# Kernel tuning notes

Measured on AMD Instinct MI355X. Metric: run time of the kernel, lower is better.

## Reference

```python
import jax, jax.numpy as jnp
import numpy as np

N_NODES = 100000
N_EDGES = 640000
D_IN = 128
D_OUT = 128
D_HID = 128  # assumed MLP hidden width (repo MLP not shown; standard 2-layer GIN MLP)


def setup_inputs() -> dict:
    key = jax.random.key(0)
    k = jax.random.split(key, 8)
    x = jax.random.normal(k[0], (N_NODES, D_IN), dtype=jnp.float32)
    edge_index = jax.random.randint(k[1], (2, N_EDGES), 0, N_NODES, dtype=jnp.int64)
    edge_attr = jax.random.normal(k[2], (N_EDGES, D_IN), dtype=jnp.float32)
    # learned params
    eps = jnp.zeros((), dtype=jnp.float32)  # train_eps=True, init 0
    s1 = 1.0 / np.sqrt(D_IN)
    s2 = 1.0 / np.sqrt(D_HID)
    W1 = jax.random.uniform(k[3], (D_IN, D_HID), jnp.float32, -s1, s1)
    b1 = jax.random.uniform(k[4], (D_HID,), jnp.float32, -s1, s1)
    W2 = jax.random.uniform(k[5], (D_HID, D_OUT), jnp.float32, -s2, s2)
    b2 = jax.random.uniform(k[6], (D_OUT,), jnp.float32, -s2, s2)
    return {"x": x, "edge_index": edge_index, "edge_attr": edge_attr,
            "eps": eps, "W1": W1, "b1": b1, "W2": W2, "b2": b2}


def reference(x, edge_index, edge_attr, eps, W1, b1, W2, b2):
    src = edge_index[0]  # source nodes j
    dst = edge_index[1]  # target nodes i
    # message: ReLU(x_j + edge_attr)  -- [E, D_IN]
    msg = jax.nn.relu(x[src] + edge_attr)
    # scatter-sum aggregation to target nodes -- [N, D_IN]
    aggr = jax.ops.segment_sum(msg, dst, num_segments=N_NODES)
    # GINE update: (1 + eps) * x_i + aggr, then MLP (dropout=0.0 -> identity)
    h = (1.0 + eps) * x + aggr
    h = jax.nn.relu(h @ W1 + b1)
    out = h @ W2 + b2
    return out
```

## Files before the change

kernel.cpp:

```cpp
#include <hip/hip_runtime.h>

constexpr int NN = 100000;
constexpr int NE = 640000;
constexpr int D  = 128;
constexpr int NB = (NN + 255) / 256;

typedef __attribute__((ext_vector_type(8))) short bf16x8;
typedef __attribute__((ext_vector_type(4))) float f32x4;

__device__ __forceinline__ short f2bf(float f) {
    union { float f; unsigned u; } v; v.f = f;
    unsigned r = v.u + 0x7FFF + ((v.u >> 16) & 1);
    return (short)(r >> 16);
}
__device__ __forceinline__ float bf2f(short h) {
    union { unsigned u; float f; } v;
    v.u = ((unsigned)(unsigned short)h) << 16;
    return v.f;
}

__global__ __launch_bounds__(256) void k_zero(int* __restrict__ cnt) {
    int i = blockIdx.x * 256 + threadIdx.x;
    if (i < NN) cnt[i] = 0;
}

__global__ __launch_bounds__(256) void k_hist(const int* __restrict__ dst,
                                              int* __restrict__ cnt) {
    int e = blockIdx.x * 256 + threadIdx.x;
    if (e < NE) atomicAdd(&cnt[dst[e]], 1);
}

__global__ __launch_bounds__(256) void k_bsum(const int* __restrict__ cnt,
                                              int* __restrict__ bsum) {
    int i = blockIdx.x * 256 + threadIdx.x;
    int v = (i < NN) ? cnt[i] : 0;
#pragma unroll
    for (int s = 32; s; s >>= 1) v += __shfl_down(v, s, 64);
    __shared__ int w[4];
    if ((threadIdx.x & 63) == 0) w[threadIdx.x >> 6] = v;
    __syncthreads();
    if (threadIdx.x == 0) bsum[blockIdx.x] = w[0] + w[1] + w[2] + w[3];
}

__global__ __launch_bounds__(512) void k_scan_bsum(const int* __restrict__ bsum,
                                                   int* __restrict__ bboff) {
    int t = threadIdx.x, lane = t & 63;
    int v = (t < NB) ? bsum[t] : 0;
    int incl = v;
#pragma unroll
    for (int s = 1; s < 64; s <<= 1) {
        int u = __shfl_up(incl, s, 64);
        if (lane >= s) incl += u;
    }
    __shared__ int wt[8], wp[8];
    if (lane == 63) wt[t >> 6] = incl;
    __syncthreads();
    if (t == 0) { int run = 0; for (int i = 0; i < 8; ++i) { wp[i] = run; run += wt[i]; } }
    __syncthreads();
    if (t < NB) bboff[t] = incl - v + wp[t >> 6];
}

__global__ __launch_bounds__(256) void k_scan_final(const int* __restrict__ cnt,
                                                    const int* __restrict__ bboff,
                                                    int* __restrict__ off,
                                                    int* __restrict__ cur) {
    int b = blockIdx.x, t = threadIdx.x, lane = t & 63;
    int i = b * 256 + t;
    int v = (i < NN) ? cnt[i] : 0;
    int incl = v;
#pragma unroll
    for (int s = 1; s < 64; s <<= 1) {
        int u = __shfl_up(incl, s, 64);
        if (lane >= s) incl += u;
    }
    __shared__ int wt[4], wp[4];
    if (lane == 63) wt[t >> 6] = incl;
    __syncthreads();
    if (t == 0) { int run = 0; for (int q = 0; q < 4; ++q) { wp[q] = run; run += wt[q]; } }
    __syncthreads();
    int excl = incl - v + wp[t >> 6] + bboff[b];
    if (i < NN) { off[i] = excl; cur[i] = excl; }
    if (i == 0) off[NN] = NE;
}

__global__ __launch_bounds__(256) void k_perm(const int* __restrict__ dst,
                                              const int* __restrict__ src,
                                              int* __restrict__ cur,
                                              int2* __restrict__ ps) {
    int e = blockIdx.x * 256 + threadIdx.x;
    if (e < NE) {
        int p = atomicAdd(&cur[dst[e]], 1);
        int2 v; v.x = e; v.y = src[e];
        ps[p] = v;
    }
}

__global__ __launch_bounds__(256) void k_agg(const float* __restrict__ x,
                                             const float* __restrict__ ea,
                                             const int* __restrict__ off,
                                             const int2* __restrict__ ps,
                                             const float* __restrict__ eps,
                                             float* __restrict__ h) {
    int wave = threadIdx.x >> 6;
    int lane = threadIdx.x & 63;
    int n = blockIdx.x * 4 + wave;
    if (n >= NN) return;
    int j0 = off[n], j1 = off[n + 1];
    const int lo2 = lane * 2;
    float2 acc; acc.x = 0.0f; acc.y = 0.0f;

    for (int j = j0; j < j1; j += 8) {
        int ee[8], ss[8];
#pragma unroll
        for (int q = 0; q < 8; ++q) {
            int jj = j + q; jj = (jj < j1) ? jj : (j1 - 1);
            int2 p = ps[jj];
            ee[q] = p.x; ss[q] = p.y;
        }
        float2 xa[8], eb[8];
#pragma unroll
        for (int q = 0; q < 8; ++q) {
            xa[q] = *reinterpret_cast<const float2*>(x  + (size_t)ss[q] * D + lo2);
            eb[q] = *reinterpret_cast<const float2*>(ea + (size_t)ee[q] * D + lo2);
        }
#pragma unroll
        for (int q = 0; q < 8; ++q) {
            float mx = fmaxf(xa[q].x + eb[q].x, 0.0f);
            float my = fmaxf(xa[q].y + eb[q].y, 0.0f);
            bool ok = (j + q) < j1;
            acc.x += ok ? mx : 0.0f;
            acc.y += ok ? my : 0.0f;
        }
    }
    float sc = 1.0f + eps[0];
    float2 xx = *reinterpret_cast<const float2*>(x + (size_t)n * D + lo2);
    float2 o;
    o.x = fmaf(sc, xx.x, acc.x);
    o.y = fmaf(sc, xx.y, acc.y);
    *reinterpret_cast<float2*>(h + (size_t)n * D + lo2) = o;
}

template<bool RELU>
__global__ __launch_bounds__(256) void k_gemm(const float* __restrict__ A,
                                              const float* __restrict__ W,
                                              const float* __restrict__ bias,
                                              float* __restrict__ out) {
    constexpr int LDW = 136;
    __shared__ short Whi[128 * LDW];
    __shared__ short Wlo[128 * LDW];

    for (int idx = threadIdx.x; idx < 128 * 128; idx += 256) {
        int k = idx >> 7, n = idx & 127;
        float w = W[idx];
        short hi = f2bf(w);
        short lo = f2bf(w - bf2f(hi));
        Whi[n * LDW + k] = hi;
        Wlo[n * LDW + k] = lo;
    }
    __syncthreads();

    const int wave = threadIdx.x >> 6;
    const int lane = threadIdx.x & 63;
    const int r = lane & 15;
    const int g = lane >> 4;

    const long mb = (long)blockIdx.x * 128 + wave * 16;

    f32x4 acc[2][8];
#pragma unroll
    for (int mt = 0; mt < 2; ++mt)
#pragma unroll
        for (int nt = 0; nt < 8; ++nt) {
            acc[mt][nt].x = 0.f; acc[mt][nt].y = 0.f;
            acc[mt][nt].z = 0.f; acc[mt][nt].w = 0.f;
        }

#pragma unroll
    for (int kc = 0; kc < 4; ++kc) {
        const int k0 = kc * 32;
        bf16x8 ahi[2], alo[2];
#pragma unroll
        for (int mt = 0; mt < 2; ++mt) {
            long row = mb + mt * 64 + r;
            row = (row < NN) ? row : (NN - 1);
            const float* ap = A + row * D + k0 + g * 8;
            float4 v0 = reinterpret_cast<const float4*>(ap)[0];
            float4 v1 = reinterpret_cast<const float4*>(ap)[1];
            float vals[8] = {v0.x, v0.y, v0.z, v0.w, v1.x, v1.y, v1.z, v1.w};
#pragma unroll
            for (int i = 0; i < 8; ++i) {
                short hb = f2bf(vals[i]);
                ahi[mt][i] = hb;
                alo[mt][i] = f2bf(vals[i] - bf2f(hb));
            }
        }
#pragma unroll
        for (int nt = 0; nt < 8; ++nt) {
            const int wb = (nt * 16 + r) * LDW + k0 + g * 8;
            bf16x8 whi = *reinterpret_cast<const bf16x8*>(&Whi[wb]);
            bf16x8 wlo = *reinterpret_cast<const bf16x8*>(&Wlo[wb]);
#pragma unroll
            for (int mt = 0; mt < 2; ++mt) {
                acc[mt][nt] = __builtin_amdgcn_mfma_f32_16x16x32_bf16(ahi[mt], whi, acc[mt][nt], 0, 0, 0);
                acc[mt][nt] = __builtin_amdgcn_mfma_f32_16x16x32_bf16(ahi[mt], wlo, acc[mt][nt], 0, 0, 0);
                acc[mt][nt] = __builtin_amdgcn_mfma_f32_16x16x32_bf16(alo[mt], whi, acc[mt][nt], 0, 0, 0);
            }
        }
    }

#pragma unroll
    for (int nt = 0; nt < 8; ++nt) {
        const int col = nt * 16 + r;
        const float bb = bias[col];
#pragma unroll
        for (int mt = 0; mt < 2; ++mt) {
#pragma unroll
            for (int q = 0; q < 4; ++q) {
                long row = mb + mt * 64 + g * 4 + q;
                if (row < NN) {
                    float v = acc[mt][nt][q] + bb;
                    if (RELU) v = fmaxf(v, 0.0f);
                    out[row * D + col] = v;
                }
            }
        }
    }
}

extern "C" void kernel_launch(void* const* d_in, const int* in_sizes, int n_in,
                              void* d_out, int out_size, void* d_ws, size_t ws_size,
                              hipStream_t stream) {
    const float* x   = (const float*)d_in[0];
    const int*   ei  = (const int*)d_in[1];
    const float* ea  = (const float*)d_in[2];
    const float* eps = (const float*)d_in[3];
    const float* W1  = (const float*)d_in[4];
    const float* b1  = (const float*)d_in[5];
    const float* W2  = (const float*)d_in[6];
    const float* b2  = (const float*)d_in[7];
    float* out = (float*)d_out;

    const int* src = ei;
    const int* dst = ei + NE;

    int* base  = (int*)d_ws;
    int* cnt   = base;
    int* off   = cnt + NN;
    int* cur   = off + NN + 1;
    int* bsum  = cur + NN;
    int* bboff = bsum + NB;
    size_t ps_off = ((size_t)(3 * NN + 1 + 2 * NB) + 1) & ~(size_t)1;
    int2* ps   = (int2*)(base + ps_off);
    float* g   = (float*)d_ws;

    k_zero      <<<NB,               256, 0, stream>>>(cnt);
    k_hist      <<<(NE + 255) / 256, 256, 0, stream>>>(dst, cnt);
    k_bsum      <<<NB,               256, 0, stream>>>(cnt, bsum);
    k_scan_bsum <<<1,                512, 0, stream>>>(bsum, bboff);
    k_scan_final<<<NB,               256, 0, stream>>>(cnt, bboff, off, cur);
    k_perm      <<<(NE + 255) / 256, 256, 0, stream>>>(dst, src, cur, ps);

    k_agg<<<(NN + 3) / 4, 256, 0, stream>>>(x, ea, off, ps, eps, out);
    k_gemm<true> <<<(NN + 127) / 128, 256, 0, stream>>>(out, W1, b1, g);
    k_gemm<false><<<(NN + 127) / 128, 256, 0, stream>>>(g, W2, b2, out);
}
```

Baseline: 305.9 us.

## Fuse two MLP GEMMs into one kernel with pre-split bf16 weights

Adds a small kernel that splits W1 and W2 once into transposed bf16 hi/lo arrays in the workspace. The two GEMM launches become one fused MLP kernel: each wave computes a 32-row slab of layer 1, stages the ReLU output in shared memory, then runs layer 2 from it. This removes the global round trip of the 100000x128 hidden activation and the per-block weight conversion into LDS. Weights are now read from global/L2 on every use instead of from shared memory. The 64KB shared buffer and two accumulator sets may lower occupancy, and A and out alias the same buffer (in place, row-local, and safe only because each wave reads its rows before writing them).

```diff
diff --git a/kernel.cpp b/kernel.cpp
--- a/kernel.cpp
+++ b/kernel.cpp
@@ -92,6 +92,18 @@
         int p = atomicAdd(&cur[dst[e]], 1);
         int2 v; v.x = e; v.y = src[e];
         ps[p] = v;
+    }
+}
+
+__global__ __launch_bounds__(256) void k_wsplit(const float* __restrict__ W,
+                                                short* __restrict__ Whi,
+                                                short* __restrict__ Wlo) {
+    for (int idx = blockIdx.x * 256 + threadIdx.x; idx < D * D; idx += gridDim.x * 256) {
+        int n = idx >> 7, k = idx & 127;
+        float w = W[k * D + n];
+        short hi = f2bf(w);
+        Whi[idx] = hi;
+        Wlo[idx] = f2bf(w - bf2f(hi));
     }
 }
 
@@ -140,39 +152,30 @@
     *reinterpret_cast<float2*>(h + (size_t)n * D + lo2) = o;
 }
 
-template<bool RELU>
-__global__ __launch_bounds__(256) void k_gemm(const float* __restrict__ A,
-                                              const float* __restrict__ W,
-                                              const float* __restrict__ bias,
+__global__ __launch_bounds__(256) void k_mlp2(const float* __restrict__ A,
+                                              const short* __restrict__ W1h,
+                                              const short* __restrict__ W1l,
+                                              const short* __restrict__ W2h,
+                                              const short* __restrict__ W2l,
+                                              const float* __restrict__ b1,
+                                              const float* __restrict__ b2,
                                               float* __restrict__ out) {
-    constexpr int LDW = 136;
-    __shared__ short Whi[128 * LDW];
-    __shared__ short Wlo[128 * LDW];
-
-    for (int idx = threadIdx.x; idx < 128 * 128; idx += 256) {
-        int k = idx >> 7, n = idx & 127;
-        float w = W[idx];
-        short hi = f2bf(w);
-        short lo = f2bf(w - bf2f(hi));
-        Whi[n * LDW + k] = hi;
-        Wlo[n * LDW + k] = lo;
-    }
-    __syncthreads();
+    __shared__ float G[4][32][D];
 
     const int wave = threadIdx.x >> 6;
     const int lane = threadIdx.x & 63;
     const int r = lane & 15;
     const int g = lane >> 4;
 
-    const long mb = (long)blockIdx.x * 128 + wave * 16;
-
-    f32x4 acc[2][8];
+    const long rb = (long)blockIdx.x * 128 + wave * 32;
+
+    f32x4 acc1[2][8];
 #pragma unroll
     for (int mt = 0; mt < 2; ++mt)
 #pragma unroll
         for (int nt = 0; nt < 8; ++nt) {
-            acc[mt][nt].x = 0.f; acc[mt][nt].y = 0.f;
-            acc[mt][nt].z = 0.f; acc[mt][nt].w = 0.f;
+            acc1[mt][nt].x = 0.f; acc1[mt][nt].y = 0.f;
+            acc1[mt][nt].z = 0.f; acc1[mt][nt].w = 0.f;
         }
 
 #pragma unroll
@@ -181,7 +184,7 @@
         bf16x8 ahi[2], alo[2];
 #pragma unroll
         for (int mt = 0; mt < 2; ++mt) {
-            long row = mb + mt * 64 + r;
+            long row = rb + mt * 16 + r;
             row = (row < NN) ? row : (NN - 1);
             const float* ap = A + row * D + k0 + g * 8;
             float4 v0 = reinterpret_cast<const float4*>(ap)[0];
@@ -196,14 +199,14 @@
         }
 #pragma unroll
         for (int nt = 0; nt < 8; ++nt) {
-            const int wb = (nt * 16 + r) * LDW + k0 + g * 8;
-            bf16x8 whi = *reinterpret_cast<const bf16x8*>(&Whi[wb]);
-            bf16x8 wlo = *reinterpret_cast<const bf16x8*>(&Wlo[wb]);
+            const int wb = (nt * 16 + r) * D + k0 + g * 8;
+            bf16x8 whi = *reinterpret_cast<const bf16x8*>(&W1h[wb]);
+            bf16x8 wlo = *reinterpret_cast<const bf16x8*>(&W1l[wb]);
 #pragma unroll
             for (int mt = 0; mt < 2; ++mt) {
-                acc[mt][nt] = __builtin_amdgcn_mfma_f32_16x16x32_bf16(ahi[mt], whi, acc[mt][nt], 0, 0, 0);
-                acc[mt][nt] = __builtin_amdgcn_mfma_f32_16x16x32_bf16(ahi[mt], wlo, acc[mt][nt], 0, 0, 0);
-                acc[mt][nt] = __builtin_amdgcn_mfma_f32_16x16x32_bf16(alo[mt], whi, acc[mt][nt], 0, 0, 0);
+                acc1[mt][nt] = __builtin_amdgcn_mfma_f32_16x16x32_bf16(ahi[mt], whi, acc1[mt][nt], 0, 0, 0);
+                acc1[mt][nt] = __builtin_amdgcn_mfma_f32_16x16x32_bf16(ahi[mt], wlo, acc1[mt][nt], 0, 0, 0);
+                acc1[mt][nt] = __builtin_amdgcn_mfma_f32_16x16x32_bf16(alo[mt], whi, acc1[mt][nt], 0, 0, 0);
             }
         }
     }
@@ -211,17 +214,68 @@
 #pragma unroll
     for (int nt = 0; nt < 8; ++nt) {
         const int col = nt * 16 + r;
-        const float bb = bias[col];
+        const float bb = b1[col];
 #pragma unroll
         for (int mt = 0; mt < 2; ++mt) {
 #pragma unroll
             for (int q = 0; q < 4; ++q) {
-                long row = mb + mt * 64 + g * 4 + q;
-                if (row < NN) {
-                    float v = acc[mt][nt][q] + bb;
-                    if (RELU) v = fmaxf(v, 0.0f);
-                    out[row * D + col] = v;
-                }
+                float v = fmaxf(acc1[mt][nt][q] + bb, 0.0f);
+                G[wave][mt * 16 + g * 4 + q][col] = v;
+            }
+        }
+    }
+    __syncthreads();
+
+    f32x4 acc2[2][8];
+#pragma unroll
+    for (int mt = 0; mt < 2; ++mt)
+#pragma unroll
+        for (int nt = 0; nt < 8; ++nt) {
+            acc2[mt][nt].x = 0.f; acc2[mt][nt].y = 0.f;
+            acc2[mt][nt].z = 0.f; acc2[mt][nt].w = 0.f;
+        }
+
+#pragma unroll
+    for (int kc = 0; kc < 4; ++kc) {
+        const int k0 = kc * 32;
+        bf16x8 ahi[2], alo[2];
+#pragma unroll
+        for (int mt = 0; mt < 2; ++mt) {
+            const float* gp = &G[wave][mt * 16 + r][k0 + g * 8];
+            float4 v0 = reinterpret_cast<const float4*>(gp)[0];
+            float4 v1 = reinterpret_cast<const float4*>(gp)[1];
+            float vals[8] = {v0.x, v0.y, v0.z, v0.w, v1.x, v1.y, v1.z, v1.w};
+#pragma unroll
+            for (int i = 0; i < 8; ++i) {
+                short hb = f2bf(vals[i]);
+                ahi[mt][i] = hb;
+                alo[mt][i] = f2bf(vals[i] - bf2f(hb));
+            }
+        }
+#pragma unroll
+        for (int nt = 0; nt < 8; ++nt) {
+            const int wb = (nt * 16 + r) * D + k0 + g * 8;
+            bf16x8 whi = *reinterpret_cast<const bf16x8*>(&W2h[wb]);
+            bf16x8 wlo = *reinterpret_cast<const bf16x8*>(&W2l[wb]);
+#pragma unroll
+            for (int mt = 0; mt < 2; ++mt) {
+                acc2[mt][nt] = __builtin_amdgcn_mfma_f32_16x16x32_bf16(ahi[mt], whi, acc2[mt][nt], 0, 0, 0);
+                acc2[mt][nt] = __builtin_amdgcn_mfma_f32_16x16x32_bf16(ahi[mt], wlo, acc2[mt][nt], 0, 0, 0);
+                acc2[mt][nt] = __builtin_amdgcn_mfma_f32_16x16x32_bf16(alo[mt], whi, acc2[mt][nt], 0, 0, 0);
+            }
+        }
+    }
+
+#pragma unroll
+    for (int nt = 0; nt < 8; ++nt) {
+        const int col = nt * 16 + r;
+        const float bb = b2[col];
+#pragma unroll
+        for (int mt = 0; mt < 2; ++mt) {
+#pragma unroll
+            for (int q = 0; q < 4; ++q) {
+                long row = rb + mt * 16 + g * 4 + q;
+                if (row < NN) out[row * D + col] = acc2[mt][nt][q] + bb;
             }
         }
     }
@@ -251,8 +305,14 @@
     int* bboff = bsum + NB;
     size_t ps_off = ((size_t)(3 * NN + 1 + 2 * NB) + 1) & ~(size_t)1;
     int2* ps   = (int2*)(base + ps_off);
-    float* g   = (float*)d_ws;
-
+    short* wsp = (short*)(base + ps_off + 2 * (size_t)NE);
+    short* W1h = wsp;
+    short* W1l = W1h + D * D;
+    short* W2h = W1l + D * D;
+    short* W2l = W2h + D * D;
+
+    k_wsplit    <<<32,               256, 0, stream>>>(W1, W1h, W1l);
+    k_wsplit    <<<32,               256, 0, stream>>>(W2, W2h, W2l);
     k_zero      <<<NB,               256, 0, stream>>>(cnt);
     k_hist      <<<(NE + 255) / 256, 256, 0, stream>>>(dst, cnt);
     k_bsum      <<<NB,               256, 0, stream>>>(cnt, bsum);
@@ -261,6 +321,5 @@
     k_perm      <<<(NE + 255) / 256, 256, 0, stream>>>(dst, src, cur, ps);
 
     k_agg<<<(NN + 3) / 4, 256, 0, stream>>>(x, ea, off, ps, eps, out);
-    k_gemm<true> <<<(NN + 127) / 128, 256, 0, stream>>>(out, W1, b1, g);
-    k_gemm<false><<<(NN + 127) / 128, 256, 0, stream>>>(g, W2, b2, out);
-}
+    k_mlp2<<<(NN + 127) / 128, 256, 0, stream>>>(out, W1h, W1l, W2h, W2l, b1, b2, out);
+}
```

New measurement: 304.6 us. Within noise of the previous version (-0.4%).
